# Kernel tuning notes

Measured on AMD Instinct MI355X. Metric: run time of the kernel, lower is better.

## Reference

```python
import jax, jax.numpy as jnp
import numpy as np
from functools import partial

A_CUBIC = -0.75  # PyTorch grid_sample bicubic coefficient

def _cubic_weights(t):
    # t in [0,1); returns 4 weights for taps at offsets -1,0,1,2
    a = A_CUBIC
    t2 = t * t; t3 = t2 * t
    w0 = a * (t3 - 2.0 * t2 + t)
    w1 = (a + 2.0) * t3 - (a + 3.0) * t2 + 1.0
    s = 1.0 - t
    w2 = (a + 2.0) * s * s * s - (a + 3.0) * s * s + 1.0
    u = 2.0 - t
    w3 = a * u * u * u - 5.0 * a * u * u + 8.0 * a * u - 4.0 * a
    return (w0, w1, w2, w3)

def grid_sample_bicubic(img, gx, gy):
    # img [N,C,H,W]; gx,gy [N,Ho,Wo] normalized coords in [-1,1]; border padding, align_corners=False
    N, C, H, W = img.shape
    ix = ((gx + 1.0) * W - 1.0) * 0.5
    iy = ((gy + 1.0) * H - 1.0) * 0.5
    x0 = jnp.floor(ix); tx = ix - x0
    y0 = jnp.floor(iy); ty = iy - y0
    x0i = x0.astype(jnp.int32); y0i = y0.astype(jnp.int32)
    wx = _cubic_weights(tx); wy = _cubic_weights(ty)
    gather = jax.vmap(lambda im, yi, xi: im[:, yi, xi])  # per-sample [C,Ho,Wo]
    out = jnp.zeros((N, C) + gx.shape[1:], img.dtype)
    for i in range(4):
        yi = jnp.clip(y0i + (i - 1), 0, H - 1)
        for j in range(4):
            xj = jnp.clip(x0i + (j - 1), 0, W - 1)
            v = gather(img, yi, xj)
            out = out + (wy[i] * wx[j])[:, None] * v
    return out

def jitter_aligned_interp(img, jitter, f):
    # F.affine_grid(identity+translation) + grid_sample bicubic, align_corners=False
    N, C, H, W = img.shape
    Ho, Wo = H * f, W * f
    bx = (2.0 * jnp.arange(Wo, dtype=img.dtype) + 1.0) / Wo - 1.0
    by = (2.0 * jnp.arange(Ho, dtype=img.dtype) + 1.0) / Ho - 1.0
    tx = 2.0 * (0.5 - jitter[:, 0]) / W
    ty = 2.0 * (0.5 - jitter[:, 1]) / H
    gx = jnp.broadcast_to(bx[None, None, :] + tx[:, None, None], (N, Ho, Wo))
    gy = jnp.broadcast_to(by[None, :, None] + ty[:, None, None], (N, Ho, Wo))
    return grid_sample_bicubic(img, gx, gy)

def zero_upsample(x, f):
    N, C, H, W = x.shape
    out = jnp.zeros((N, C, H * f, W * f), x.dtype)
    return out.at[:, :, ::f, ::f].set(x)

def jitter_align(img, jitter, f):
    # pad by f, per-sample crop at integer jitter offset (zero constant pad)
    N, C, H, W = img.shape
    ji = jnp.floor(jitter * f).astype(jnp.int32)  # [N,2] (x,y)
    padded = jnp.pad(img, ((0, 0), (0, 0), (f, f), (f, f)))
    def crop(im, j):
        sy = f - j[1]; sx = f - j[0]
        return jax.lax.dynamic_slice(im, (0, sy, sx), (C, H, W))
    return jax.vmap(crop)(padded, ji)

def resize_bilinear(x, f):
    # F.interpolate bilinear, align_corners=False (half-pixel, clamp to >=0 and edges)
    N, C, H, W = x.shape
    def coords(L):
        c = jnp.maximum((jnp.arange(L * f, dtype=x.dtype) + 0.5) / f - 0.5, 0.0)
        i0 = jnp.floor(c); t = c - i0
        i0 = i0.astype(jnp.int32)
        return jnp.clip(i0, 0, L - 1), jnp.clip(i0 + 1, 0, L - 1), t
    y0, y1, tyv = coords(H)
    x0, x1, txv = coords(W)
    xr = x[:, :, y0, :] * (1.0 - tyv)[None, None, :, None] + x[:, :, y1, :] * tyv[None, None, :, None]
    return xr[:, :, :, x0] * (1.0 - txv) + xr[:, :, :, x1] * txv

def conv3x3_reppad(x, w, b):
    x = jnp.pad(x, ((0, 0), (0, 0), (1, 1), (1, 1)), mode='edge')
    y = jax.lax.conv_general_dilated(x, w, (1, 1), 'VALID',
                                     dimension_numbers=('NCHW', 'OIHW', 'NCHW'))
    return y + b[None, :, None, None]

def sub_forward(frame, depth, mv, jitter, history, params, f):
    w1, b1, w2, b2, w3, b3 = params
    N = frame.shape[0]
    far, near = 100.0, 0.1
    d = near * far / (far - depth * (far - near))
    d = (d - near) / (far - near)
    frame4 = jnp.concatenate([frame, d], axis=1)  # [N,4,H,W]
    frame_bicubic = jitter_aligned_interp(frame4, jitter, f)  # [N,4,Hf,Wf]
    frame_up = jitter_align(zero_upsample(frame4, f), jitter, f)
    if history is None:
        history = frame_bicubic
    else:
        mv_hi = resize_bilinear(jnp.moveaxis(mv, 3, 1), f)       # [N,2,Hf,Wf]
        mv_hi = jnp.moveaxis(mv_hi, 1, 3)                        # [N,Hf,Wf,2]
        history = grid_sample_bicubic(history, mv_hi[..., 0], mv_hi[..., 1])
        oob = jnp.logical_or(mv_hi > 1.0, mv_hi < -1.0)
        mask = jnp.logical_or(oob[..., 0], oob[..., 1])[:, None]  # [N,1,Hf,Wf]
        history = jnp.where(mask, frame_bicubic, history)
    cnn_in = jnp.concatenate([frame_up, history], axis=1)  # [N,8,Hf,Wf]
    h = jax.nn.relu(conv3x3_reppad(cnn_in, w1, b1))
    h = jax.nn.relu(conv3x3_reppad(h, w2, b2))
    residual = conv3x3_reppad(h, w3, b3)  # [N,2,Hf,Wf]
    alpha = jnp.clip(residual[:, 0:1], 0.0, 1.0)
    history = history * (1.0 - alpha) + frame_bicubic * alpha
    history = jnp.concatenate([history[:, :3], history[:, 3:4] + residual[:, 1:2]], axis=1)
    history = jnp.clip(history, 0.0, 1.0)
    return history[:, :3], history

FACTOR = 2

def setup_inputs() -> dict:
    key = jax.random.key(0)
    ks = jax.random.split(key, 10)
    T, N, H, W = 3, 2, 360, 640
    frames = jax.random.uniform(ks[0], (T, N, 3, H, W), jnp.float32)
    depths = jax.random.uniform(ks[1], (T, N, 1, H, W), jnp.float32)
    mvs = jax.random.uniform(ks[2], (T, N, H, W, 2), jnp.float32, -1.05, 1.05)
    jitters = jax.random.uniform(ks[3], (T, N, 2), jnp.float32)
    w1 = jax.random.normal(ks[4], (64, 8, 3, 3), jnp.float32) * 0.1
    b1 = jnp.zeros((64,), jnp.float32)
    w2 = jax.random.normal(ks[5], (64, 64, 3, 3), jnp.float32) * 0.04
    b2 = jnp.zeros((64,), jnp.float32)
    w3 = jax.random.normal(ks[6], (2, 64, 3, 3), jnp.float32) * 0.04
    b3 = jnp.zeros((2,), jnp.float32)
    return {"frames": frames, "depths": depths, "mvs": mvs, "jitters": jitters,
            "w1": w1, "b1": b1, "w2": w2, "b2": b2, "w3": w3, "b3": b3}

def reference(frames, depths, mvs, jitters, w1, b1, w2, b2, w3, b3):
    params = (w1, b1, w2, b2, w3, b3)
    T = frames.shape[0]
    history = None
    outs = []
    for t in range(T - 1, -1, -1):  # torch forward iterates seq_length-1 .. 0
        recon, history = sub_forward(frames[t], depths[t], mvs[t], jitters[t], history, params, FACTOR)
        outs.append(recon)
    outs.reverse()
    return jnp.stack(outs)  # [T,N,3,H*f,W*f]
```

## Files before the change

### kernel.cpp

```cpp
#include <hip/hip_runtime.h>

#define T_STEPS 3
#define NB 2
#define H_LO 360
#define W_LO 640
#define H_HI 720
#define W_HI 1280
#define HW_LO (H_LO*W_LO)
#define HW_HI (H_HI*W_HI)
#define TILE 12

typedef _Float16 f16;
typedef __attribute__((ext_vector_type(4))) _Float16 f16x4;
typedef __attribute__((ext_vector_type(8))) _Float16 f16x8;
typedef __attribute__((ext_vector_type(4))) float f32x4;

#define OFF_H1  0
#define OFF_H2  0
#define OFF_CNN 32768
#define OFF_RES 32768
#define LDS_BYTES 37952

__device__ __forceinline__ int imin(int a,int b){return a<b?a:b;}
__device__ __forceinline__ int imax(int a,int b){return a>b?a:b;}
__device__ __forceinline__ int iclamp(int v,int lo,int hi){return imin(imax(v,lo),hi);}

__device__ __forceinline__ float depth_tx(float d0){
  float d = 10.0f / (100.0f - d0*99.9f);
  return (d - 0.1f) / 99.9f;
}

__device__ __forceinline__ void cubw(float t, float* w){
  const float a = -0.75f;
  float t2 = t*t, t3 = t2*t;
  w[0] = a*(t3 - 2.0f*t2 + t);
  w[1] = (a+2.0f)*t3 - (a+3.0f)*t2 + 1.0f;
  float s = 1.0f - t;
  w[2] = (a+2.0f)*s*s*s - (a+3.0f)*s*s + 1.0f;
  float u = 2.0f - t;
  w[3] = a*u*u*u - 5.0f*a*u*u + 8.0f*a*u - 4.0f*a;
}

__global__ __launch_bounds__(256) void k_prep(const float* __restrict__ frame,
    const float* __restrict__ depth, const float* __restrict__ jit,
    float4* __restrict__ FB){
  int idx = blockIdx.x*256 + threadIdx.x;
  if (idx >= NB*HW_HI) return;
  int n = idx / HW_HI, p = idx - n*HW_HI;
  int y = p / W_HI, x = p - y*W_HI;
  float jx = jit[n*2], jy = jit[n*2+1];
  float gx = (2.0f*(float)x + 1.0f)/(float)W_HI - 1.0f + 2.0f*(0.5f - jx)/(float)W_LO;
  float gy = (2.0f*(float)y + 1.0f)/(float)H_HI - 1.0f + 2.0f*(0.5f - jy)/(float)H_LO;
  float ix = ((gx + 1.0f)*(float)W_LO - 1.0f)*0.5f;
  float iy = ((gy + 1.0f)*(float)H_LO - 1.0f)*0.5f;
  float xf = floorf(ix), yf = floorf(iy);
  float tx = ix - xf, ty = iy - yf;
  int xi = (int)xf, yi = (int)yf;
  float wx[4], wy[4]; cubw(tx, wx); cubw(ty, wy);
  int xs[4], ys[4];
  #pragma unroll
  for (int j=0;j<4;j++){ xs[j]=iclamp(xi-1+j,0,W_LO-1); ys[j]=iclamp(yi-1+j,0,H_LO-1); }
  const float* fb = frame + (size_t)n*3*HW_LO;
  const float* db = depth + (size_t)n*HW_LO;
  float a0=0.f,a1=0.f,a2=0.f,a3=0.f;
  #pragma unroll
  for (int i=0;i<4;i++){
    #pragma unroll
    for (int j=0;j<4;j++){
      float wgt = wy[i]*wx[j];
      int off = ys[i]*W_LO + xs[j];
      a0 += wgt*fb[off];
      a1 += wgt*fb[HW_LO+off];
      a2 += wgt*fb[2*HW_LO+off];
      a3 += wgt*depth_tx(db[off]);
    }
  }
  FB[(size_t)n*HW_HI + p] = make_float4(a0,a1,a2,a3);
}

__global__ __launch_bounds__(256) void k_wprep(const float* __restrict__ w1g,
    const float* __restrict__ w2g, const float* __restrict__ w3g, f16* __restrict__ wbuf){
  int i = blockIdx.x*256 + threadIdx.x;
  if (i >= 46592) return;
  float val = 0.0f;
  if (i < 8192){
    int oc = i>>7, kk = i&127, k = kk ^ ((oc&7)<<3);
    if (k < 72) val = w1g[(oc*8 + (k&7))*9 + (k>>3)];
  } else if (i < 45056){
    int j = i - 8192; int oc = j/576, kk = j - oc*576, k = kk ^ ((oc&7)<<3);
    val = w2g[(oc*64 + (k&63))*9 + (k>>6)];
  } else {
    int j = i - 45056;
    if (j < 1152){ int nn = j/576, k = j - nn*576;
      val = w3g[(nn*64 + (k&63))*9 + (k>>6)];
    }
  }
  wbuf[i] = (f16)val;
}

__global__ __launch_bounds__(256) void k_warp(const float4* __restrict__ histA,
    const float* __restrict__ mv, const float4* __restrict__ FB,
    float4* __restrict__ histB){
  int idx = blockIdx.x*256 + threadIdx.x;
  if (idx >= NB*HW_HI) return;
  int n = idx / HW_HI, p = idx - n*HW_HI;
  int y = p / W_HI, x = p - y*W_HI;
  float cy = fmaxf(((float)y + 0.5f)/2.0f - 0.5f, 0.0f);
  float cx = fmaxf(((float)x + 0.5f)/2.0f - 0.5f, 0.0f);
  float y0f = floorf(cy), x0f = floorf(cx);
  float tyv = cy - y0f, txv = cx - x0f;
  int y0 = iclamp((int)y0f, 0, H_LO-1), y1 = iclamp((int)y0f+1, 0, H_LO-1);
  int x0 = iclamp((int)x0f, 0, W_LO-1), x1 = iclamp((int)x0f+1, 0, W_LO-1);
  const float* mb = mv + (size_t)n*HW_LO*2;
  float gx, gy;
  {
    float v00 = mb[(y0*W_LO+x0)*2], v01 = mb[(y0*W_LO+x1)*2];
    float v10 = mb[(y1*W_LO+x0)*2], v11 = mb[(y1*W_LO+x1)*2];
    float r0 = v00*(1.0f-tyv) + v10*tyv;
    float r1 = v01*(1.0f-tyv) + v11*tyv;
    gx = r0*(1.0f-txv) + r1*txv;
  }
  {
    float v00 = mb[(y0*W_LO+x0)*2+1], v01 = mb[(y0*W_LO+x1)*2+1];
    float v10 = mb[(y1*W_LO+x0)*2+1], v11 = mb[(y1*W_LO+x1)*2+1];
    float r0 = v00*(1.0f-tyv) + v10*tyv;
    float r1 = v01*(1.0f-tyv) + v11*tyv;
    gy = r0*(1.0f-txv) + r1*txv;
  }
  bool oob = (gx > 1.0f) || (gx < -1.0f) || (gy > 1.0f) || (gy < -1.0f);
  float4 res;
  if (oob) {
    res = FB[(size_t)n*HW_HI + p];
  } else {
    const float4* hb = histA + (size_t)n*HW_HI;
    float ix = ((gx + 1.0f)*(float)W_HI - 1.0f)*0.5f;
    float iy = ((gy + 1.0f)*(float)H_HI - 1.0f)*0.5f;
    float xf = floorf(ix), yf = floorf(iy);
    float tx = ix - xf, ty = iy - yf;
    int xi = (int)xf, yi = (int)yf;
    float wx[4], wy[4]; cubw(tx, wx); cubw(ty, wy);
    int xs[4], ys[4];
    #pragma unroll
    for (int j=0;j<4;j++){ xs[j]=iclamp(xi-1+j,0,W_HI-1); ys[j]=iclamp(yi-1+j,0,H_HI-1); }
    float a0=0.f,a1=0.f,a2=0.f,a3=0.f;
    #pragma unroll
    for (int i=0;i<4;i++){
      #pragma unroll
      for (int j=0;j<4;j++){
        float wgt = wy[i]*wx[j];
        float4 v = hb[ys[i]*W_HI + xs[j]];
        a0 += wgt*v.x; a1 += wgt*v.y; a2 += wgt*v.z; a3 += wgt*v.w;
      }
    }
    res = make_float4(a0,a1,a2,a3);
  }
  histB[(size_t)n*HW_HI + p] = res;
}

__global__ __launch_bounds__(256,3) void k_fused(
    const float* __restrict__ frame, const float* __restrict__ depth,
    const float* __restrict__ jit, const float4* __restrict__ histIn,
    const float4* __restrict__ FB, const f16* __restrict__ wbuf,
    const float* __restrict__ b1g, const float* __restrict__ b2g, const float* __restrict__ b3g,
    float4* __restrict__ histOut, float* __restrict__ outp)
{
  __shared__ __attribute__((aligned(16))) char smem[LDS_BYTES];
  const int tid = threadIdx.x;
  const int wv = tid>>6, ln = tid&63, lr = ln&15, lq = ln>>4;
  const int n  = blockIdx.z;
  const int r0 = blockIdx.y * TILE;
  const int c0 = blockIdx.x * TILE;
  const float jx = jit[n*2], jy = jit[n*2+1];
  const int jix = (int)floorf(jx*2.0f), jiy = (int)floorf(jy*2.0f);
  const float* fbase = frame + (size_t)n*3*HW_LO;
  const float* dbase = depth + (size_t)n*HW_LO;
  const float4* hist4 = histIn + (size_t)n*HW_HI;
  const int wkk = (lr&7)<<3;

  f16x8 B1[3][4];
  #pragma unroll
  for (int kc=0;kc<3;kc++)
    #pragma unroll
    for (int oct=0;oct<4;oct++){
      int oc = oct*16 + lr;
      int k0 = kc*32 + lq*8;
      B1[kc][oct] = *(const f16x8*)(wbuf + oc*128 + (k0 ^ wkk));
    }

  for (int e=tid; e<324; e+=256){
    int u = e/18, v = e - u*18;
    int cgy = iclamp(r0-3+u, 0, H_HI-1);
    int cgx = iclamp(c0-3+v, 0, W_HI-1);
    float v0=0.f, v1=0.f, v2=0.f, v3=0.f;
    int yy = cgy - jiy, xx = cgx - jix;
    if (yy>=0 && xx>=0 && !(yy&1) && !(xx&1)){
      int off = (yy>>1)*W_LO + (xx>>1);
      v0 = fbase[off]; v1 = fbase[HW_LO+off]; v2 = fbase[2*HW_LO+off];
      v3 = depth_tx(dbase[off]);
    }
    float4 h = hist4[cgy*W_HI + cgx];
    f16x8 pk;
    pk[0]=(f16)v0; pk[1]=(f16)v1; pk[2]=(f16)v2; pk[3]=(f16)v3;
    pk[4]=(f16)h.x; pk[5]=(f16)h.y; pk[6]=(f16)h.z; pk[7]=(f16)h.w;
    *(f16x8*)(smem + OFF_CNN + e*16) = pk;
  }
  __syncthreads();

  {
    float4 b1v[4];
    #pragma unroll
    for (int oct=0;oct<4;oct++) b1v[oct] = *(const float4*)(b1g + oct*16 + lq*4);
    #pragma unroll
    for (int ty4=0;ty4<4;ty4++){
      int ty = wv*4 + ty4;
      int g1y = iclamp(r0-2+ty, 0, H_HI-1);
      int g1x = iclamp(c0-2+lr, 0, W_HI-1);
      f32x4 acc[4];
      #pragma unroll
      for (int oct=0;oct<4;oct++) acc[oct] = (f32x4){b1v[oct].x,b1v[oct].y,b1v[oct].z,b1v[oct].w};
      #pragma unroll
      for (int kc=0;kc<3;kc++){
        int k0 = kc*32 + lq*8;
        int t = imin(k0>>3, 8);
        int dy = (t*11)>>5; int dx = t - dy*3;
        int uu = iclamp(g1y+dy-1, 0, H_HI-1) - (r0-3);
        int vv = iclamp(g1x+dx-1, 0, W_HI-1) - (c0-3);
        f16x8 a = *(const f16x8*)(smem + OFF_CNN + (uu*18+vv)*16);
        #pragma unroll
        for (int oct=0;oct<4;oct++)
          acc[oct] = __builtin_amdgcn_mfma_f32_16x16x32_f16(B1[kc][oct], a, acc[oct], 0,0,0);
      }
      #pragma unroll
      for (int oct=0;oct<4;oct++){
        f16x4 wv4;
        #pragma unroll
        for (int reg=0;reg<4;reg++) wv4[reg] = (f16)fmaxf(acc[oct][reg], 0.f);
        int oc0 = (oct*16 + lq*4) ^ ((lr&7)<<3);
        *(f16x4*)(smem + OFF_H1 + (((ty*16+lr)*64 + oc0)<<1)) = wv4;
      }
    }
  }
  __syncthreads();

  {
    const int nmt = (wv==0) ? 4 : 3;
    const int mtid[4] = {wv, 4+wv, 8+wv, 12};
    int rowOf[4][3], colc[4][3][2];
    #pragma unroll
    for (int mti=0;mti<4;mti++){
      int m = imin(mtid[mti]*16 + lr, 195);
      int py = m/14, px = m - py*14;
      int Ay = iclamp(r0-1+py, 0, H_HI-1);
      int Ax = iclamp(c0-1+px, 0, W_HI-1);
      #pragma unroll
      for (int d=0;d<3;d++){
        rowOf[mti][d] = (iclamp(Ay+d-1, 0, H_HI-1) - (r0-2))*1024;
        int vv = iclamp(Ax+d-1, 0, W_HI-1) - (c0-2);
        int key = (vv&7)<<3;
        colc[mti][d][0] = vv*64 + ((lq*8) ^ key);
        colc[mti][d][1] = vv*64 + ((32+lq*8) ^ key);
      }
    }
    float4 b2v[4];
    #pragma unroll
    for (int oct=0;oct<4;oct++) b2v[oct] = *(const float4*)(b2g + oct*16 + lq*4);
    f32x4 acc2[4][4];
    #pragma unroll
    for (int mti=0;mti<4;mti++)
      #pragma unroll
      for (int oct=0;oct<4;oct++) acc2[mti][oct] = (f32x4){b2v[oct].x,b2v[oct].y,b2v[oct].z,b2v[oct].w};
    const f16* w2b = wbuf + 8192;
    f16x8 bf[4];
    #pragma unroll
    for (int oct=0;oct<4;oct++)
      bf[oct] = *(const f16x8*)(w2b + (oct*16+lr)*576 + ((lq*8) ^ wkk));
    #pragma unroll
    for (int kc=0;kc<18;kc++){
      const int tap = kc>>1, half = kc&1;
      const int dy = tap/3, dx = tap - dy*3;
      f16x8 bfn[4];
      if (kc < 17){
        const int kn = kc+1, tapn = kn>>1, halfn = kn&1;
        #pragma unroll
        for (int oct=0;oct<4;oct++)
          bfn[oct] = *(const f16x8*)(w2b + (oct*16+lr)*576 + ((tapn*64 + halfn*32 + lq*8) ^ wkk));
      }
      #pragma unroll
      for (int mti=0;mti<4;mti++) if (mti < nmt){
        f16x8 a = *(const f16x8*)(smem + OFF_H1 + ((rowOf[mti][dy] + colc[mti][dx][half])<<1));
        #pragma unroll
        for (int oct=0;oct<4;oct++)
          acc2[mti][oct] = __builtin_amdgcn_mfma_f32_16x16x32_f16(bf[oct], a, acc2[mti][oct], 0,0,0);
      }
      #pragma unroll
      for (int oct=0;oct<4;oct++) bf[oct] = bfn[oct];
    }
    __syncthreads();
    #pragma unroll
    for (int mti=0;mti<4;mti++) if (mti < nmt){
      int m = mtid[mti]*16 + lr;
      if (m < 196){
        int py = m/14, px = m - py*14;
        int base = (py*14+px)*64; int key = (px&7)<<3;
        #pragma unroll
        for (int oct=0;oct<4;oct++){
          f16x4 wv4;
          #pragma unroll
          for (int reg=0;reg<4;reg++) wv4[reg] = (f16)fmaxf(acc2[mti][oct][reg], 0.f);
          *(f16x4*)(smem + OFF_H2 + ((base + ((oct*16 + lq*4) ^ key))<<1)) = wv4;
        }
      }
    }
  }
  __syncthreads();

  {
    const int nm3 = (wv==0) ? 3 : 2;
    const int m3t[3] = {wv, 4+wv, 8};
    int rowOf[3][3], colc[3][3][2];
    #pragma unroll
    for (int i=0;i<3;i++){
      int m = m3t[i]*16 + lr;
      int py = m/12, px = m - py*12;
      int Cy = r0 + py;
      int Cx = iclamp(c0+px, 0, W_HI-1);
      #pragma unroll
      for (int d=0;d<3;d++){
        rowOf[i][d] = (iclamp(Cy+d-1, 0, H_HI-1) - (r0-1))*896;
        int vv = iclamp(Cx+d-1, 0, W_HI-1) - (c0-1);
        int key = (vv&7)<<3;
        colc[i][d][0] = vv*64 + ((lq*8) ^ key);
        colc[i][d][1] = vv*64 + ((32+lq*8) ^ key);
      }
    }
    f32x4 acc3[3] = {{0,0,0,0},{0,0,0,0},{0,0,0,0}};
    const int cidx = ln&1;
    const f16* w3b = wbuf + 45056;
    f16x8 b = *(const f16x8*)(w3b + cidx*576 + lq*8);
    #pragma unroll
    for (int kc=0;kc<18;kc++){
      const int tap = kc>>1, half = kc&1;
      const int dy = tap/3, dx = tap - dy*3;
      f16x8 bn;
      if (kc < 17) bn = *(const f16x8*)(w3b + cidx*576 + (kc+1)*32 + lq*8);
      #pragma unroll
      for (int i=0;i<3;i++) if (i < nm3){
        f16x8 a = *(const f16x8*)(smem + OFF_H2 + ((rowOf[i][dy] + colc[i][dx][half])<<1));
        acc3[i] = __builtin_amdgcn_mfma_f32_16x16x32_f16(a, b, acc3[i], 0,0,0);
      }
      b = bn;
    }
    __syncthreads();
    float* sres = (float*)(smem + OFF_RES);
    if (lr < 2){
      float bv = b3g[lr];
      #pragma unroll
      for (int i=0;i<3;i++) if (i < nm3){
        #pragma unroll
        for (int reg=0;reg<4;reg++){
          int m = m3t[i]*16 + lq*4 + reg;
          sres[lr*144 + m] = acc3[i][reg] + bv;
        }
      }
    }
  }
  __syncthreads();

  if (tid < 144){
    int ty = tid/12, tx = tid - ty*12;
    int gy = r0 + ty, gx = c0 + tx;
    if (gx < W_HI){
      const float* sres = (const float*)(smem + OFF_RES);
      float a0 = sres[tid], a1 = sres[144+tid];
      float alpha = fminf(fmaxf(a0, 0.0f), 1.0f);
      int pix = gy*W_HI + gx;
      float4 fb = FB[(size_t)n*HW_HI + pix];
      float4 hv = hist4[pix];
      float h0 = hv.x*(1.0f-alpha) + fb.x*alpha;
      float h1 = hv.y*(1.0f-alpha) + fb.y*alpha;
      float h2 = hv.z*(1.0f-alpha) + fb.z*alpha;
      float h3 = hv.w*(1.0f-alpha) + fb.w*alpha + a1;
      h0 = fminf(fmaxf(h0,0.f),1.f); h1 = fminf(fmaxf(h1,0.f),1.f);
      h2 = fminf(fmaxf(h2,0.f),1.f); h3 = fminf(fmaxf(h3,0.f),1.f);
      histOut[(size_t)n*HW_HI + pix] = make_float4(h0,h1,h2,h3);
      float* rp = outp + (size_t)n*3*HW_HI + pix;
      rp[0] = h0; rp[HW_HI] = h1; rp[2*HW_HI] = h2;
    }
  }
}

extern "C" void kernel_launch(void* const* d_in, const int* in_sizes, int n_in,
                              void* d_out, int out_size, void* d_ws, size_t ws_size,
                              hipStream_t stream){
  const float* frames = (const float*)d_in[0];
  const float* depths = (const float*)d_in[1];
  const float* mvs    = (const float*)d_in[2];
  const float* jits   = (const float*)d_in[3];
  const float* w1 = (const float*)d_in[4];
  const float* b1 = (const float*)d_in[5];
  const float* w2 = (const float*)d_in[6];
  const float* b2 = (const float*)d_in[7];
  const float* w3 = (const float*)d_in[8];
  const float* b3 = (const float*)d_in[9];
  float* out = (float*)d_out;

  float4* FB4 = (float4*)d_ws;
  float4* HA  = FB4 + (size_t)NB*HW_HI;
  float4* HB  = HA  + (size_t)NB*HW_HI;
  f16*  wbuf = (f16*)(HB + (size_t)NB*HW_HI);

  dim3 bs(256);
  int npix = NB*HW_HI;
  dim3 gpix((npix + 255)/256);
  dim3 gfused((W_HI + TILE-1)/TILE, (H_HI + TILE-1)/TILE, NB);

  k_wprep<<<dim3((46592+255)/256), bs, 0, stream>>>(w1, w2, w3, wbuf);

  for (int t = T_STEPS-1; t >= 0; --t){
    const float* fr = frames + (size_t)t*NB*3*HW_LO;
    const float* dp = depths + (size_t)t*NB*HW_LO;
    const float* mv = mvs    + (size_t)t*NB*HW_LO*2;
    const float* jt = jits   + (size_t)t*NB*2;
    float* ot = out + (size_t)t*NB*3*HW_HI;

    k_prep<<<gpix, bs, 0, stream>>>(fr, dp, jt, FB4);
    const float4* histIn;
    if (t == T_STEPS-1) {
      histIn = FB4;
    } else {
      k_warp<<<gpix, bs, 0, stream>>>(HA, mv, FB4, HB);
      histIn = HB;
    }
    k_fused<<<gfused, bs, 0, stream>>>(fr, dp, jt, histIn, FB4, wbuf,
        b1, b2, b3, HA, ot);
  }
}
```

Measured before the change: 1.339 ms.

## Fuse bicubic prep into warp kernel and raise fused-kernel occupancy

Merges the frame/depth bicubic upsampling kernel into the history-warp kernel, so the FB value is computed in registers and reused on the out-of-bounds path instead of being written and read back. This saves one launch and one global re-read per step. Also drops the weight-buffer XOR swizzle and the software-prefetched B-operand double buffering in the conv MFMA loops, which lowers register pressure so launch_bounds can go from 3 to 4 waves per SIMD. The trade-off is loss of the prefetch overlap and possible bank conflicts on the unswizzled weight reads.

```diff
diff --git a/kernel.cpp b/kernel.cpp
--- a/kernel.cpp
+++ b/kernel.cpp
@@ -41,14 +41,8 @@
   w[3] = a*u*u*u - 5.0f*a*u*u + 8.0f*a*u - 4.0f*a;
 }
 
-__global__ __launch_bounds__(256) void k_prep(const float* __restrict__ frame,
-    const float* __restrict__ depth, const float* __restrict__ jit,
-    float4* __restrict__ FB){
-  int idx = blockIdx.x*256 + threadIdx.x;
-  if (idx >= NB*HW_HI) return;
-  int n = idx / HW_HI, p = idx - n*HW_HI;
-  int y = p / W_HI, x = p - y*W_HI;
-  float jx = jit[n*2], jy = jit[n*2+1];
+__device__ __forceinline__ float4 fb_bicubic(const float* __restrict__ fbase,
+    const float* __restrict__ dbase, float jx, float jy, int x, int y){
   float gx = (2.0f*(float)x + 1.0f)/(float)W_HI - 1.0f + 2.0f*(0.5f - jx)/(float)W_LO;
   float gy = (2.0f*(float)y + 1.0f)/(float)H_HI - 1.0f + 2.0f*(0.5f - jy)/(float)H_LO;
   float ix = ((gx + 1.0f)*(float)W_LO - 1.0f)*0.5f;
@@ -60,8 +54,6 @@
   int xs[4], ys[4];
   #pragma unroll
   for (int j=0;j<4;j++){ xs[j]=iclamp(xi-1+j,0,W_LO-1); ys[j]=iclamp(yi-1+j,0,H_LO-1); }
-  const float* fb = frame + (size_t)n*3*HW_LO;
-  const float* db = depth + (size_t)n*HW_LO;
   float a0=0.f,a1=0.f,a2=0.f,a3=0.f;
   #pragma unroll
   for (int i=0;i<4;i++){
@@ -69,13 +61,13 @@
     for (int j=0;j<4;j++){
       float wgt = wy[i]*wx[j];
       int off = ys[i]*W_LO + xs[j];
-      a0 += wgt*fb[off];
-      a1 += wgt*fb[HW_LO+off];
-      a2 += wgt*fb[2*HW_LO+off];
-      a3 += wgt*depth_tx(db[off]);
-    }
-  }
-  FB[(size_t)n*HW_HI + p] = make_float4(a0,a1,a2,a3);
+      a0 += wgt*fbase[off];
+      a1 += wgt*fbase[HW_LO+off];
+      a2 += wgt*fbase[2*HW_LO+off];
+      a3 += wgt*depth_tx(dbase[off]);
+    }
+  }
+  return make_float4(a0,a1,a2,a3);
 }
 
 __global__ __launch_bounds__(256) void k_wprep(const float* __restrict__ w1g,
@@ -84,11 +76,11 @@
   if (i >= 46592) return;
   float val = 0.0f;
   if (i < 8192){
-    int oc = i>>7, kk = i&127, k = kk ^ ((oc&7)<<3);
-    if (k < 72) val = w1g[(oc*8 + (k&7))*9 + (k>>3)];
+    int oc = i>>7, kk = i&127;
+    if (kk < 72) val = w1g[(oc*8 + (kk&7))*9 + (kk>>3)];
   } else if (i < 45056){
-    int j = i - 8192; int oc = j/576, kk = j - oc*576, k = kk ^ ((oc&7)<<3);
-    val = w2g[(oc*64 + (k&63))*9 + (k>>6)];
+    int j = i - 8192; int oc = j/576, kk = j - oc*576;
+    val = w2g[(oc*64 + (kk&63))*9 + (kk>>6)];
   } else {
     int j = i - 45056;
     if (j < 1152){ int nn = j/576, k = j - nn*576;
@@ -98,13 +90,20 @@
   wbuf[i] = (f16)val;
 }
 
-__global__ __launch_bounds__(256) void k_warp(const float4* __restrict__ histA,
-    const float* __restrict__ mv, const float4* __restrict__ FB,
-    float4* __restrict__ histB){
+__global__ __launch_bounds__(256) void k_pw(const float4* __restrict__ histA,
+    const float* __restrict__ mv, const float* __restrict__ frame,
+    const float* __restrict__ depth, const float* __restrict__ jit,
+    float4* __restrict__ FB, float4* __restrict__ histB, int doWarp){
   int idx = blockIdx.x*256 + threadIdx.x;
   if (idx >= NB*HW_HI) return;
   int n = idx / HW_HI, p = idx - n*HW_HI;
   int y = p / W_HI, x = p - y*W_HI;
+  const float* fbase = frame + (size_t)n*3*HW_LO;
+  const float* dbase = depth + (size_t)n*HW_LO;
+  float4 fb4 = fb_bicubic(fbase, dbase, jit[n*2], jit[n*2+1], x, y);
+  FB[(size_t)n*HW_HI + p] = fb4;
+  if (!doWarp) return;
+
   float cy = fmaxf(((float)y + 0.5f)/2.0f - 0.5f, 0.0f);
   float cx = fmaxf(((float)x + 0.5f)/2.0f - 0.5f, 0.0f);
   float y0f = floorf(cy), x0f = floorf(cx);
@@ -130,7 +129,7 @@
   bool oob = (gx > 1.0f) || (gx < -1.0f) || (gy > 1.0f) || (gy < -1.0f);
   float4 res;
   if (oob) {
-    res = FB[(size_t)n*HW_HI + p];
+    res = fb4;
   } else {
     const float4* hb = histA + (size_t)n*HW_HI;
     float ix = ((gx + 1.0f)*(float)W_HI - 1.0f)*0.5f;
@@ -157,7 +156,7 @@
   histB[(size_t)n*HW_HI + p] = res;
 }
 
-__global__ __launch_bounds__(256,3) void k_fused(
+__global__ __launch_bounds__(256,4) void k_fused(
     const float* __restrict__ frame, const float* __restrict__ depth,
     const float* __restrict__ jit, const float4* __restrict__ histIn,
     const float4* __restrict__ FB, const f16* __restrict__ wbuf,
@@ -175,17 +174,13 @@
   const float* fbase = frame + (size_t)n*3*HW_LO;
   const float* dbase = depth + (size_t)n*HW_LO;
   const float4* hist4 = histIn + (size_t)n*HW_HI;
-  const int wkk = (lr&7)<<3;
 
   f16x8 B1[3][4];
   #pragma unroll
   for (int kc=0;kc<3;kc++)
     #pragma unroll
-    for (int oct=0;oct<4;oct++){
-      int oc = oct*16 + lr;
-      int k0 = kc*32 + lq*8;
-      B1[kc][oct] = *(const f16x8*)(wbuf + oc*128 + (k0 ^ wkk));
-    }
+    for (int oct=0;oct<4;oct++)
+      B1[kc][oct] = *(const f16x8*)(wbuf + (oct*16+lr)*128 + kc*32 + lq*8);
 
   for (int e=tid; e<324; e+=256){
     int u = e/18, v = e - u*18;
@@ -245,7 +240,7 @@
   {
     const int nmt = (wv==0) ? 4 : 3;
     const int mtid[4] = {wv, 4+wv, 8+wv, 12};
-    int rowOf[4][3], colc[4][3][2];
+    int rowOf[4][3], colc[4][3];
     #pragma unroll
     for (int mti=0;mti<4;mti++){
       int m = imin(mtid[mti]*16 + lr, 195);
@@ -256,9 +251,7 @@
       for (int d=0;d<3;d++){
         rowOf[mti][d] = (iclamp(Ay+d-1, 0, H_HI-1) - (r0-2))*1024;
         int vv = iclamp(Ax+d-1, 0, W_HI-1) - (c0-2);
-        int key = (vv&7)<<3;
-        colc[mti][d][0] = vv*64 + ((lq*8) ^ key);
-        colc[mti][d][1] = vv*64 + ((32+lq*8) ^ key);
+        colc[mti][d] = vv*64 + ((lq*8) ^ ((vv&7)<<3));
       }
     }
     float4 b2v[4];
@@ -270,30 +263,21 @@
       #pragma unroll
       for (int oct=0;oct<4;oct++) acc2[mti][oct] = (f32x4){b2v[oct].x,b2v[oct].y,b2v[oct].z,b2v[oct].w};
     const f16* w2b = wbuf + 8192;
-    f16x8 bf[4];
-    #pragma unroll
-    for (int oct=0;oct<4;oct++)
-      bf[oct] = *(const f16x8*)(w2b + (oct*16+lr)*576 + ((lq*8) ^ wkk));
     #pragma unroll
     for (int kc=0;kc<18;kc++){
       const int tap = kc>>1, half = kc&1;
       const int dy = tap/3, dx = tap - dy*3;
-      f16x8 bfn[4];
-      if (kc < 17){
-        const int kn = kc+1, tapn = kn>>1, halfn = kn&1;
-        #pragma unroll
-        for (int oct=0;oct<4;oct++)
-          bfn[oct] = *(const f16x8*)(w2b + (oct*16+lr)*576 + ((tapn*64 + halfn*32 + lq*8) ^ wkk));
-      }
+      f16x8 bf[4];
+      #pragma unroll
+      for (int oct=0;oct<4;oct++)
+        bf[oct] = *(const f16x8*)(w2b + (oct*16+lr)*576 + tap*64 + half*32 + lq*8);
       #pragma unroll
       for (int mti=0;mti<4;mti++) if (mti < nmt){
-        f16x8 a = *(const f16x8*)(smem + OFF_H1 + ((rowOf[mti][dy] + colc[mti][dx][half])<<1));
+        f16x8 a = *(const f16x8*)(smem + OFF_H1 + ((rowOf[mti][dy] + (colc[mti][dx] ^ (half<<5)))<<1));
         #pragma unroll
         for (int oct=0;oct<4;oct++)
           acc2[mti][oct] = __builtin_amdgcn_mfma_f32_16x16x32_f16(bf[oct], a, acc2[mti][oct], 0,0,0);
       }
-      #pragma unroll
-      for (int oct=0;oct<4;oct++) bf[oct] = bfn[oct];
     }
     __syncthreads();
     #pragma unroll
@@ -317,7 +301,7 @@
   {
     const int nm3 = (wv==0) ? 3 : 2;
     const int m3t[3] = {wv, 4+wv, 8};
-    int rowOf[3][3], colc[3][3][2];
+    int rowOf[3][3], colc[3][3];
     #pragma unroll
     for (int i=0;i<3;i++){
       int m = m3t[i]*16 + lr;
@@ -328,27 +312,22 @@
       for (int d=0;d<3;d++){
         rowOf[i][d] = (iclamp(Cy+d-1, 0, H_HI-1) - (r0-1))*896;
         int vv = iclamp(Cx+d-1, 0, W_HI-1) - (c0-1);
-        int key = (vv&7)<<3;
-        colc[i][d][0] = vv*64 + ((lq*8) ^ key);
-        colc[i][d][1] = vv*64 + ((32+lq*8) ^ key);
+        colc[i][d] = vv*64 + ((lq*8) ^ ((vv&7)<<3));
       }
     }
     f32x4 acc3[3] = {{0,0,0,0},{0,0,0,0},{0,0,0,0}};
     const int cidx = ln&1;
     const f16* w3b = wbuf + 45056;
-    f16x8 b = *(const f16x8*)(w3b + cidx*576 + lq*8);
     #pragma unroll
     for (int kc=0;kc<18;kc++){
       const int tap = kc>>1, half = kc&1;
       const int dy = tap/3, dx = tap - dy*3;
-      f16x8 bn;
-      if (kc < 17) bn = *(const f16x8*)(w3b + cidx*576 + (kc+1)*32 + lq*8);
+      f16x8 b = *(const f16x8*)(w3b + cidx*576 + kc*32 + lq*8);
       #pragma unroll
       for (int i=0;i<3;i++) if (i < nm3){
-        f16x8 a = *(const f16x8*)(smem + OFF_H2 + ((rowOf[i][dy] + colc[i][dx][half])<<1));
+        f16x8 a = *(const f16x8*)(smem + OFF_H2 + ((rowOf[i][dy] + (colc[i][dx] ^ (half<<5)))<<1));
         acc3[i] = __builtin_amdgcn_mfma_f32_16x16x32_f16(a, b, acc3[i], 0,0,0);
       }
-      b = bn;
     }
     __syncthreads();
     float* sres = (float*)(smem + OFF_RES);
@@ -422,15 +401,10 @@
     const float* mv = mvs    + (size_t)t*NB*HW_LO*2;
     const float* jt = jits   + (size_t)t*NB*2;
     float* ot = out + (size_t)t*NB*3*HW_HI;
-
-    k_prep<<<gpix, bs, 0, stream>>>(fr, dp, jt, FB4);
-    const float4* histIn;
-    if (t == T_STEPS-1) {
-      histIn = FB4;
-    } else {
-      k_warp<<<gpix, bs, 0, stream>>>(HA, mv, FB4, HB);
-      histIn = HB;
-    }
+    int doWarp = (t != T_STEPS-1) ? 1 : 0;
+
+    k_pw<<<gpix, bs, 0, stream>>>(HA, mv, fr, dp, jt, FB4, HB, doWarp);
+    const float4* histIn = doWarp ? (const float4*)HB : (const float4*)FB4;
     k_fused<<<gfused, bs, 0, stream>>>(fr, dp, jt, histIn, FB4, wbuf,
         b1, b2, b3, HA, ot);
   }
```

Measured after the change: 2.112 ms. 1.58x slower.
